# Kernel optimization log

Measured on AMD Instinct MI355X. Metric: run time of the kernel, lower is better.

The kernel has to match this reference:

```python
import jax, jax.numpy as jnp
import numpy as np

ALIGN_CORNERS = True   # module init arg
NUM_AUX = 8            # auxiliary samples for linearized multi-sampling
NOISE_STRENGTH = 0.5   # noise scale in units of input pixel spacing
EPS = 1e-6             # Tikhonov term for the per-pixel 2x2 least squares


def _base_coords(n, align_corners):
    if align_corners:
        return jnp.linspace(-1.0, 1.0, n, dtype=jnp.float32)
    return (jnp.arange(n, dtype=jnp.float32) * 2.0 + 1.0) / n - 1.0


def affine_grid(theta, h_out, w_out, align_corners):
    # theta: [B,2,3] -> grid [B,h_out,w_out,2] with (x,y) in [-1,1]
    xs = _base_coords(w_out, align_corners)
    ys = _base_coords(h_out, align_corners)
    X, Y = jnp.meshgrid(xs, ys)                      # [H,W]
    base = jnp.stack([X, Y, jnp.ones_like(X)], -1)   # [H,W,3]
    return jnp.einsum('hwk,bik->bhwi', base, theta)  # [B,H,W,2]


def bilinear_sample(image, grid, align_corners):
    # image [B,C,Hi,Wi], grid [B,H,W,2] -> [B,H,W,C], zero padding outside
    B, C, Hi, Wi = image.shape
    x, y = grid[..., 0], grid[..., 1]
    if align_corners:
        ix = (x + 1.0) * 0.5 * (Wi - 1)
        iy = (y + 1.0) * 0.5 * (Hi - 1)
    else:
        ix = ((x + 1.0) * Wi - 1.0) * 0.5
        iy = ((y + 1.0) * Hi - 1.0) * 0.5
    x0 = jnp.floor(ix); y0 = jnp.floor(iy)
    wx1 = ix - x0; wy1 = iy - y0
    bidx = jnp.arange(B)[:, None, None]

    def tap(xi, yi, w):
        valid = (xi >= 0) & (xi <= Wi - 1) & (yi >= 0) & (yi <= Hi - 1)
        xc = jnp.clip(xi, 0, Wi - 1).astype(jnp.int32)
        yc = jnp.clip(yi, 0, Hi - 1).astype(jnp.int32)
        v = image[bidx, :, yc, xc]                   # [B,H,W,C] gather
        return v * (w * valid)[..., None]

    return (tap(x0, y0, (1 - wx1) * (1 - wy1)) +
            tap(x0 + 1, y0, wx1 * (1 - wy1)) +
            tap(x0, y0 + 1, (1 - wx1) * wy1) +
            tap(x0 + 1, y0 + 1, wx1 * wy1))


def linearized_grid_sample(image, grid, align_corners):
    # Linearized multi-sampling (Jiang et al., ICCV'19): forward value equals
    # the center bilinear sample; gradient wrt grid flows through a per-pixel
    # least-squares linearization fitted from NUM_AUX noisy auxiliary samples.
    B, C, Hi, Wi = image.shape
    key = jax.random.key(42)
    spacing = jnp.array([2.0 / Wi, 2.0 / Hi], dtype=jnp.float32)  # one input pixel in norm coords
    g0 = jax.lax.stop_gradient(grid)
    noise = jax.random.normal(key, (B, NUM_AUX) + grid.shape[1:3] + (2,), dtype=jnp.float32)
    aux = g0[:, None] + noise * NOISE_STRENGTH * spacing          # [B,K,H,W,2]

    center = bilinear_sample(image, g0, align_corners)            # [B,H,W,C]
    samp = jax.vmap(lambda g: bilinear_sample(image, g, align_corners),
                    in_axes=1, out_axes=1)(aux)                   # [B,K,H,W,C]

    d_int = samp - center[:, None]                                # [B,K,H,W,C]
    d_grid = aux - g0[:, None]                                    # [B,K,H,W,2]
    xtx = jnp.einsum('bkhwi,bkhwj->bhwij', d_grid, d_grid) \
        + EPS * jnp.eye(2, dtype=jnp.float32)                     # [B,H,W,2,2]
    xty = jnp.einsum('bkhwi,bkhwc->bhwic', d_grid, d_int)         # [B,H,W,2,C]
    slope = jnp.linalg.solve(xtx, xty)                            # [B,H,W,2,C]

    out = center + jnp.einsum('bhwic,bhwi->bhwc', slope, grid - g0)
    return jnp.transpose(out, (0, 3, 1, 2))                       # [B,C,H,W]


def setup_inputs() -> dict:
    key = jax.random.key(0)
    k1, k2 = jax.random.split(key)
    B, C, Hi, Wi = 4, 3, 1024, 1024
    image = jax.random.normal(k1, (B, C, Hi, Wi), dtype=jnp.float32)
    ident = jnp.tile(jnp.array([[1.0, 0.0, 0.0], [0.0, 1.0, 0.0]], dtype=jnp.float32), (B, 1, 1))
    pMtrx = ident + 0.05 * jax.random.normal(k2, (B, 2, 3), dtype=jnp.float32)
    return {"image": image, "pMtrx": pMtrx, "W": 1024, "H": 1024}


def reference(image, pMtrx, W, H):
    # torch.affine_grid_generator(pMtrx, (B,3,W,H)) -> grid [B, W, H, 2]
    grid = affine_grid(pMtrx, W, H, ALIGN_CORNERS)
    return linearized_grid_sample(image, grid, ALIGN_CORNERS)  # [B,C,W,H]
```

## Files before the change

kernel.cpp:

```cpp
#include <hip/hip_runtime.h>


#define B_  4
#define C_  3
#define HI  1024
#define WI  1024
#define HO  1024
#define WO  1024

#define TW  32
#define TH  16
#define BANDW 52
#define BANDH 32
#define NSEG (BANDW/4)
#define LDS_CH (BANDH * BANDW)

typedef float vf4 __attribute__((ext_vector_type(4)));

__device__ __forceinline__ float2 map_px(int w, int h,
                                         float t0, float t1, float t2,
                                         float t3, float t4, float t5) {
    const float xs = -1.0f + 2.0f * (float)w / (float)(WO - 1);
    const float ys = -1.0f + 2.0f * (float)h / (float)(HO - 1);
    const float x = t0 * xs + (t1 * ys + t2);
    const float y = t3 * xs + (t4 * ys + t5);
    const float ix = (x + 1.0f) * 0.5f * (float)(WI - 1);
    const float iy = (y + 1.0f) * 0.5f * (float)(HI - 1);
    return make_float2(ix, iy);
}

__global__ __launch_bounds__(256) void warp_bilinear_tile_kernel(
    const float* __restrict__ image,
    const float* __restrict__ theta,
    float* __restrict__ out)
{
    __shared__ float lds[C_ * LDS_CH];

    const int bid = blockIdx.x;
    const int b   = bid >> 11;
    const int rem = bid & 2047;
    const int h0  = (rem >> 5) * TH;
    const int w0  = (rem & 31) * TW;

    const float* t = theta + b * 6;
    const float t0 = t[0], t1 = t[1], t2 = t[2];
    const float t3 = t[3], t4 = t[4], t5 = t[5];

    const float2 c00 = map_px(w0,        h0,        t0,t1,t2,t3,t4,t5);
    const float2 c10 = map_px(w0+TW-1,   h0,        t0,t1,t2,t3,t4,t5);
    const float2 c01 = map_px(w0,        h0+TH-1,   t0,t1,t2,t3,t4,t5);
    const float2 c11 = map_px(w0+TW-1,   h0+TH-1,   t0,t1,t2,t3,t4,t5);

    const float ixmin = fminf(fminf(c00.x, c10.x), fminf(c01.x, c11.x));
    const float iymin = fminf(fminf(c00.y, c10.y), fminf(c01.y, c11.y));

    int bx = (int)floorf(ixmin) - 1;
    bx = min(max(bx, 0), WI - BANDW);
    bx &= ~3;
    int by = (int)floorf(iymin) - 1;
    by = min(max(by, 0), HI - BANDH);

    const float* imgb = image + (size_t)b * (C_ * HI * WI);

#pragma unroll 2
    for (int i = threadIdx.x; i < C_ * BANDH * NSEG; i += 256) {
        const int c   = i / (BANDH * NSEG);
        const int rr  = i - c * (BANDH * NSEG);
        const int r   = rr / NSEG;
        const int seg = rr - r * NSEG;
        const vf4 v = *(const vf4*)(imgb + c * (HI * WI) + (by + r) * WI + bx + seg * 4);
        *(vf4*)(lds + c * LDS_CH + r * BANDW + seg * 4) = v;
    }
    __syncthreads();

    const int wloc = threadIdx.x & 31;
    const int ty   = threadIdx.x >> 5;
    const int w    = w0 + wloc;

    float* ob = out + (size_t)b * (C_ * HO * WO) + w;

#pragma unroll
    for (int k = 0; k < 2; ++k) {
        const int h = h0 + ty + 8 * k;

        const float2 ixy = map_px(w, h, t0, t1, t2, t3, t4, t5);
        const float ix = ixy.x, iy = ixy.y;

        const float x0f = floorf(ix);
        const float y0f = floorf(iy);
        const float wx1 = ix - x0f;
        const float wy1 = iy - y0f;
        const int x0 = (int)x0f;
        const int y0 = (int)y0f;

        const float ax0 = (1.0f - wx1) * ((x0 >= 0 && x0 <= WI - 1) ? 1.0f : 0.0f);
        const float ax1 = wx1          * ((x0 >= -1 && x0 <= WI - 2) ? 1.0f : 0.0f);
        const float ay0 = (1.0f - wy1) * ((y0 >= 0 && y0 <= HI - 1) ? 1.0f : 0.0f);
        const float ay1 = wy1          * ((y0 >= -1 && y0 <= HI - 2) ? 1.0f : 0.0f);

        const float w00 = ax0 * ay0, w10 = ax1 * ay0;
        const float w01 = ax0 * ay1, w11 = ax1 * ay1;

        const int xl0 = min(max(min(max(x0,     0), WI - 1) - bx, 0), BANDW - 1);
        const int xl1 = min(max(min(max(x0 + 1, 0), WI - 1) - bx, 0), BANDW - 1);
        const int yl0 = min(max(min(max(y0,     0), HI - 1) - by, 0), BANDH - 1);
        const int yl1 = min(max(min(max(y0 + 1, 0), HI - 1) - by, 0), BANDH - 1);

        const int o00 = yl0 * BANDW + xl0;
        const int o10 = yl0 * BANDW + xl1;
        const int o01 = yl1 * BANDW + xl0;
        const int o11 = yl1 * BANDW + xl1;

#pragma unroll
        for (int c = 0; c < C_; ++c) {
            const float* p = lds + c * LDS_CH;
            const float v = p[o00] * w00 + p[o10] * w10
                          + p[o01] * w01 + p[o11] * w11;
            __builtin_nontemporal_store(v, ob + c * (HO * WO) + h * WO);
        }
    }
}

extern "C" void kernel_launch(void* const* d_in, const int* in_sizes, int n_in,
                              void* d_out, int out_size, void* d_ws, size_t ws_size,
                              hipStream_t stream) {
    const float* image = (const float*)d_in[0];
    const float* theta = (const float*)d_in[1];
    float* out = (float*)d_out;

    const int grid = B_ * (HO / TH) * (WO / TW);
    warp_bilinear_tile_kernel<<<grid, 256, 0, stream>>>(image, theta, out);
}
```

Measured before the change: 117.7 us.

## Use direct global-to-LDS DMA loads and taller tiles for the warp sampler

```diff
diff --git a/kernel.cpp b/kernel.cpp
--- a/kernel.cpp
+++ b/kernel.cpp
@@ -9,13 +9,17 @@
 #define WO  1024
 
 #define TW  32
-#define TH  16
+#define TH  32
 #define BANDW 52
-#define BANDH 32
-#define NSEG (BANDW/4)
+#define BANDH 48
+#define NSEG  13
+#define SEGS_CH (BANDH * NSEG)
+#define SEGS_TOT (C_ * SEGS_CH)
 #define LDS_CH (BANDH * BANDW)
+#define NITER ((SEGS_TOT + 63) / 64)
 
-typedef float vf4 __attribute__((ext_vector_type(4)));
+typedef __attribute__((address_space(3))) void* lds_vp;
+typedef const __attribute__((address_space(1))) void* gbl_vp;
 
 __device__ __forceinline__ float2 map_px(int w, int h,
                                          float t0, float t1, float t2,
@@ -29,16 +33,16 @@
     return make_float2(ix, iy);
 }
 
-__global__ __launch_bounds__(256) void warp_bilinear_tile_kernel(
+__global__ __launch_bounds__(256) void warp_bilinear_dma_kernel(
     const float* __restrict__ image,
     const float* __restrict__ theta,
     float* __restrict__ out)
 {
-    __shared__ float lds[C_ * LDS_CH];
+    __shared__ float lds[NITER * 256];
 
     const int bid = blockIdx.x;
-    const int b   = bid >> 11;
-    const int rem = bid & 2047;
+    const int b   = bid >> 10;
+    const int rem = bid & 1023;
     const int h0  = (rem >> 5) * TH;
     const int w0  = (rem & 31) * TW;
 
@@ -62,26 +66,32 @@
 
     const float* imgb = image + (size_t)b * (C_ * HI * WI);
 
-#pragma unroll 2
-    for (int i = threadIdx.x; i < C_ * BANDH * NSEG; i += 256) {
-        const int c   = i / (BANDH * NSEG);
-        const int rr  = i - c * (BANDH * NSEG);
-        const int r   = rr / NSEG;
-        const int seg = rr - r * NSEG;
-        const vf4 v = *(const vf4*)(imgb + c * (HI * WI) + (by + r) * WI + bx + seg * 4);
-        *(vf4*)(lds + c * LDS_CH + r * BANDW + seg * 4) = v;
+    const int wv   = threadIdx.x >> 6;
+    const int lane = threadIdx.x & 63;
+#pragma unroll
+    for (int j = wv; j < NITER; j += 4) {
+        const int seg = j * 64 + lane;
+        if (seg < SEGS_TOT) {
+            const int c  = seg / SEGS_CH;
+            const int r2 = seg - c * SEGS_CH;
+            const int r  = r2 / NSEG;
+            const int s  = r2 - r * NSEG;
+            const float* gp = imgb + c * (HI * WI) + (by + r) * WI + (bx + s * 4);
+            __builtin_amdgcn_global_load_lds((gbl_vp)gp, (lds_vp)(lds + j * 256),
+                                             16, 0, 0);
+        }
     }
     __syncthreads();
 
     const int wloc = threadIdx.x & 31;
-    const int ty   = threadIdx.x >> 5;
+    const int tyq  = threadIdx.x >> 5;
     const int w    = w0 + wloc;
 
     float* ob = out + (size_t)b * (C_ * HO * WO) + w;
 
 #pragma unroll
-    for (int k = 0; k < 2; ++k) {
-        const int h = h0 + ty + 8 * k;
+    for (int k = 0; k < 4; ++k) {
+        const int h = h0 + tyq + 8 * k;
 
         const float2 ixy = map_px(w, h, t0, t1, t2, t3, t4, t5);
         const float ix = ixy.x, iy = ixy.y;
@@ -129,5 +139,5 @@
     float* out = (float*)d_out;
 
     const int grid = B_ * (HO / TH) * (WO / TW);
-    warp_bilinear_tile_kernel<<<grid, 256, 0, stream>>>(image, theta, out);
+    warp_bilinear_dma_kernel<<<grid, 256, 0, stream>>>(image, theta, out);
 }
```

After: 115.0 us. -2.3%, faster.
